# Performance work log

Hardware: AMD Instinct MI355X
Metric: run time of the kernel (lower is better)

## Reference

```python
import jax, jax.numpy as jnp
import numpy as np

SEG_LENS = (2048, 4096, 8192)
DIL_RATES = (1, 2, 4)
NUM_HEADS = 12
HEAD_DIM = 64
LN_EPS = 1e-5


def _dilated_attention(q, k, v):
    # q,k,v: [b, n, h, d]; heads partitioned across (segment, dilation) groups
    b, n, h, d = q.shape
    G = len(SEG_LENS)
    hg = h // G
    scale = d ** -0.5
    out = jnp.zeros_like(q)
    for i, (s, r) in enumerate(zip(SEG_LENS, DIL_RATES)):
        hmin = i * hg
        m = n // s                      # number of segments
        idx = jnp.arange(i % r, s, r)   # dilated positions within a segment, len = s // r
        def seg(t):
            # [b, n, hg, d] -> [b, m, s//r, hg, d]
            return t[:, :, hmin:hmin + hg, :].reshape(b, m, s, hg, d)[:, :, idx]
        qs, ks, vs = seg(q), seg(k), seg(v)
        scores = jnp.einsum('bmshd,bmthd->bmhst', qs, ks) * scale  # [b,m,hg,s/r,s/r]
        attn = jax.nn.softmax(scores, axis=-1)
        o = jnp.einsum('bmhst,bmthd->bmshd', attn, vs)              # [b,m,s/r,hg,d]
        pos = (jnp.arange(m)[:, None] * s + idx[None, :]).reshape(-1)
        out = out.at[:, pos, hmin:hmin + hg, :].set(o.reshape(b, -1, hg, d))
    return out


def setup_inputs() -> dict:
    key = jax.random.key(0)
    ks = jax.random.split(key, 4)
    E = NUM_HEADS * HEAD_DIM
    b, n = 1, 8192
    x = jax.random.normal(ks[0], (b, n, E), dtype=jnp.float32)
    w_qkv = jax.random.normal(ks[1], (3 * E, E), dtype=jnp.float32) * (E ** -0.5)
    b_qkv = jnp.zeros((3 * E,), dtype=jnp.float32)
    w_out = jax.random.normal(ks[2], (E, E), dtype=jnp.float32) * (E ** -0.5)
    b_out = jnp.zeros((E,), dtype=jnp.float32)
    ln_gamma = jnp.ones((E,), dtype=jnp.float32)
    ln_beta = jnp.zeros((E,), dtype=jnp.float32)
    return {'x': x, 'w_qkv': w_qkv, 'b_qkv': b_qkv, 'w_out': w_out,
            'b_out': b_out, 'ln_gamma': ln_gamma, 'ln_beta': ln_beta}


def reference(x, w_qkv, b_qkv, w_out, b_out, ln_gamma, ln_beta):
    b, n, E = x.shape
    qkv = x @ w_qkv.T + b_qkv
    q, k, v = jnp.split(qkv, 3, axis=-1)
    shp = (b, n, NUM_HEADS, HEAD_DIM)
    o = _dilated_attention(q.reshape(shp), k.reshape(shp), v.reshape(shp)).reshape(b, n, E)
    # MAGNETO: LayerNorm on attention output before out projection
    mu = jnp.mean(o, axis=-1, keepdims=True)
    var = jnp.mean(jnp.square(o - mu), axis=-1, keepdims=True)
    on = (o - mu) / jnp.sqrt(var + LN_EPS) * ln_gamma + ln_beta
    return on @ w_out.T + b_out
```

## Files before the change

### kernel.cpp

```cpp
#include <hip/hip_runtime.h>
#include <hip/hip_bf16.h>
#include <cstdint>
#include <cstddef>


typedef __attribute__((ext_vector_type(8))) short short8;
typedef __attribute__((ext_vector_type(4))) short short4_;
typedef __attribute__((ext_vector_type(4))) float float4_;
typedef __attribute__((ext_vector_type(16))) float floatx16;
typedef __attribute__((ext_vector_type(4))) int int4_;

#if __has_builtin(__builtin_amdgcn_exp2f)
#define EXP2(x) __builtin_amdgcn_exp2f(x)
#else
#define EXP2(x) exp2f(x)
#endif

__device__ __forceinline__ float bf2f(short s) {
    unsigned int u = ((unsigned int)(unsigned short)s) << 16;
    float f;
    __builtin_memcpy(&f, &u, 4);
    return f;
}
__device__ __forceinline__ short f2bf(float f) {
    unsigned int u;
    __builtin_memcpy(&u, &f, 4);
    u += 0x7fffu + ((u >> 16) & 1u);
    return (short)(u >> 16);
}
__device__ __forceinline__ short8 f8_to_bf8(const float* __restrict__ p) {
    float4_ a = *(const float4_*)(p);
    float4_ b = *(const float4_*)(p + 4);
    short8 r;
    r[0] = f2bf(a[0]); r[1] = f2bf(a[1]); r[2] = f2bf(a[2]); r[3] = f2bf(a[3]);
    r[4] = f2bf(b[0]); r[5] = f2bf(b[1]); r[6] = f2bf(b[2]); r[7] = f2bf(b[3]);
    return r;
}
__device__ __forceinline__ void gll16(const short* g, short* l) {
    __builtin_amdgcn_global_load_lds(
        (const __attribute__((address_space(1))) unsigned int*)g,
        (__attribute__((address_space(3))) unsigned int*)l, 16, 0, 0);
}
__device__ __forceinline__ int cvtpk(float lo, float hi) {
    int r;
    asm("v_cvt_pk_bf16_f32 %0, %1, %2" : "=v"(r) : "v"(lo), "v"(hi));
    return r;
}

#define LDT 72

__global__ __launch_bounds__(256) void cvt3(
    const float* __restrict__ a, int na, const float* __restrict__ b, int nb,
    const float* __restrict__ c, int nc,
    short* __restrict__ oa, short* __restrict__ ob, short* __restrict__ oc)
{
    int i = (blockIdx.x * 256 + threadIdx.x) * 8;
    if (i < na) {
        *(short8*)&oa[i] = f8_to_bf8(a + i);
    } else if (i < na + nb) {
        int j = i - na;
        *(short8*)&ob[j] = f8_to_bf8(b + j);
    } else {
        int j = i - na - nb;
        if (j < nc) *(short8*)&oc[j] = f8_to_bf8(c + j);
    }
}

template<int EPI>
__global__ __launch_bounds__(256) void gemm128(
    const short* __restrict__ A, int lda,
    const short* __restrict__ B,
    const float* __restrict__ bias,
    void* __restrict__ Cv,
    int N, int K)
{
    __shared__ short As[128 * 64];
    __shared__ short Bs[128 * 64];
    const int tid  = threadIdx.x;
    const int wave = tid >> 6, lane = tid & 63;
    const int quad = lane >> 4, l16 = lane & 15;
    const int wr = wave >> 1, wc = wave & 1;
    const int m0 = blockIdx.y * 128, n0 = blockIdx.x * 128;
    const int lrow   = lane >> 3;
    const int lchunk = (lane & 7) ^ lrow;

    const short* Abase = A + (size_t)(m0 + wave * 32 + lrow) * lda + lchunk * 8;
    const short* Bbase = B + (size_t)(n0 + wave * 32 + lrow) * (size_t)K + lchunk * 8;
    short* AsW = &As[(wave * 32) * 64];
    short* BsW = &Bs[(wave * 32) * 64];

    float4_ acc[4][4] = {};

    for (int k0 = 0; k0 < K; k0 += 64) {
        __syncthreads();
        #pragma unroll
        for (int i = 0; i < 4; i++) {
            gll16(Abase + (size_t)(i * 8) * lda + k0, AsW + (i * 8) * 64);
            gll16(Bbase + (size_t)(i * 8) * K   + k0, BsW + (i * 8) * 64);
        }
        __syncthreads();
        #pragma unroll
        for (int ks = 0; ks < 2; ks++) {
            short8 af[4], bf[4];
            const int ca = ((ks * 4 + quad) ^ (l16 & 7)) * 8;
            #pragma unroll
            for (int t = 0; t < 4; t++) {
                af[t] = *(const short8*)&As[(wr * 64 + t * 16 + l16) * 64 + ca];
                bf[t] = *(const short8*)&Bs[(wc * 64 + t * 16 + l16) * 64 + ca];
            }
            #pragma unroll
            for (int mt = 0; mt < 4; mt++)
                #pragma unroll
                for (int nt = 0; nt < 4; nt++)
                    acc[mt][nt] = __builtin_amdgcn_mfma_f32_16x16x32_bf16(
                        af[mt], bf[nt], acc[mt][nt], 0, 0, 0);
        }
    }

    #pragma unroll
    for (int nt = 0; nt < 4; nt++) {
        const int col = n0 + wc * 64 + nt * 16 + l16;
        const float bv = bias[col];
        if constexpr (EPI == 0) {
            short* C = (short*)Cv;
            const int g = col >> 8;
            #pragma unroll
            for (int mt = 0; mt < 4; mt++) {
                #pragma unroll
                for (int r = 0; r < 4; r++) {
                    int row = m0 + wr * 64 + mt * 16 + quad * 4 + r;
                    bool cov = (col >= 768) || (g == 0) ||
                               (g == 1 && (row & 1) == 1) ||
                               (g == 2 && (row & 3) == 2);
                    C[(size_t)row * N + col] = cov ? f2bf(acc[mt][nt][r] + bv) : (short)0;
                }
            }
        } else {
            float* C = (float*)Cv;
            #pragma unroll
            for (int mt = 0; mt < 4; mt++)
                #pragma unroll
                for (int r = 0; r < 4; r++) {
                    int row = m0 + wr * 64 + mt * 16 + quad * 4 + r;
                    C[(size_t)row * N + col] = acc[mt][nt][r] + bv;
                }
        }
    }
}

__global__ __launch_bounds__(256, 3) void dilated_attn(
    short* __restrict__ qkv, float* __restrict__ lbuf)
{
    __shared__ short Ks[2 * 64 * 64];
    __shared__ short Vt[2 * 64 * LDT];

    const int bx = blockIdx.x;
    const int L  = (bx & 7) * 56 + (bx >> 3);
    const int qt = L & 15;
    const int sh = L >> 4;

    int g, seg, s, rate, off0;
    if (sh < 16)      { g = 0; seg = sh >> 2;        s = 2048; rate = 1; off0 = 0; }
    else if (sh < 24) { g = 1; seg = (sh - 16) >> 2; s = 4096; rate = 2; off0 = 1; }
    else              { g = 2; seg = 0;              s = 8192; rate = 4; off0 = 2; }
    const int head = g * 4 + (sh & 3);

    const int tid  = threadIdx.x;
    const int wave = tid >> 6, lane = tid & 63;
    const int h = lane >> 5, l32 = lane & 31;
    const int srow = tid >> 2, scol = (tid & 3) * 16;

    const size_t bpos = (size_t)seg * s + off0
                      + (size_t)(qt * 128 + wave * 32) * rate;
    short8 aq[4];
    {
        const short* qsrc = qkv + (bpos + (size_t)l32 * rate) * 2304
                                + head * 64 + h * 8;
        #pragma unroll
        for (int kt = 0; kt < 4; kt++) {
            short8 q = *(const short8*)(qsrc + kt * 16);
            #pragma unroll
            for (int e = 0; e < 8; e++) q[e] = f2bf(bf2f(q[e]) * 0.1803368801111244f);
            aq[kt] = q;
        }
    }

    const int krow0  = wave * 8 + (lane >> 3);
    const int kchunk = (lane & 7) ^ (lane >> 3);
    const size_t kstep = (size_t)64 * rate * 2304;
    const short* kg0 = qkv + ((size_t)seg * s + off0 + (size_t)krow0 * rate) * 2304
                           + 768 + head * 64 + kchunk * 8;
    const short* kg1 = kg0 + (size_t)32 * rate * 2304;
    const short* vgp = qkv + ((size_t)seg * s + off0 + (size_t)srow * rate) * 2304
                           + 1536 + head * 64 + scol;
    const int kofsA = (wave * 8) * 64;
    const int kofsB = kofsA + 32 * 64;
    const int vswz  = scol;

    gll16(kg0, &Ks[kofsA]);
    gll16(kg1, &Ks[kofsB]);
    kg0 += kstep; kg1 += kstep;
    short8 va0 = *(const short8*)(vgp);
    short8 va1 = *(const short8*)(vgp + 8);
    vgp += kstep;
    #pragma unroll
    for (int e = 0; e < 8; e++) Vt[(scol + e) * LDT + (srow ^ vswz)] = va0[e];
    #pragma unroll
    for (int e = 0; e < 8; e++) Vt[(scol + 8 + e) * LDT + (srow ^ vswz)] = va1[e];
    va0 = *(const short8*)(vgp);
    va1 = *(const short8*)(vgp + 8);
    vgp += kstep;

    float lsum = 0.f;
    floatx16 oacc[2] = {};

    for (int j = 0; j < 32; j++) {
        __syncthreads();
        if (j < 31) {
            const int nb = (j + 1) & 1;
            gll16(kg0, &Ks[nb * 4096 + kofsA]);
            gll16(kg1, &Ks[nb * 4096 + kofsB]);
            kg0 += kstep; kg1 += kstep;
            short* vt = &Vt[nb * 64 * LDT];
            #pragma unroll
            for (int e = 0; e < 8; e++) vt[(scol + e) * LDT + (srow ^ vswz)] = va0[e];
            #pragma unroll
            for (int e = 0; e < 8; e++) vt[(scol + 8 + e) * LDT + (srow ^ vswz)] = va1[e];
            if (j < 30) {
                va0 = *(const short8*)(vgp);
                va1 = *(const short8*)(vgp + 8);
                vgp += kstep;
            }
        }
        const short* kb = &Ks[(j & 1) * 4096];
        const short* vb = &Vt[(j & 1) * 64 * LDT];

        floatx16 sacc[2] = {};
        __builtin_amdgcn_s_setprio(1);
        #pragma unroll
        for (int kt = 0; kt < 4; kt++) {
            #pragma unroll
            for (int t = 0; t < 2; t++) {
                short8 ak = *(const short8*)&kb[(t * 32 + l32) * 64
                                                + (((kt * 2 + h) ^ (l32 & 7)) * 8)];
                sacc[t] = __builtin_amdgcn_mfma_f32_32x32x16_bf16(
                    ak, aq[kt], sacc[t], 0, 0, 0);
            }
        }
        __builtin_amdgcn_s_setprio(0);

        #pragma unroll
        for (int e = 0; e < 16; e++) {
            float pa_ = EXP2(sacc[0][e]);
            float pb_ = EXP2(sacc[1][e]);
            sacc[0][e] = pa_; sacc[1][e] = pb_;
            lsum += pa_ + pb_;
        }

        short8 pa[4];
        #pragma unroll
        for (int kt = 0; kt < 4; kt++) {
            const int t = kt >> 1, b = (kt & 1) * 8;
            int A1 = cvtpk(sacc[t][b + 0], sacc[t][b + 1]);
            int A2 = cvtpk(sacc[t][b + 2], sacc[t][b + 3]);
            int B1 = cvtpk(sacc[t][b + 4], sacc[t][b + 5]);
            int B2 = cvtpk(sacc[t][b + 6], sacc[t][b + 7]);
            asm volatile("v_permlane32_swap_b32 %0, %1" : "+v"(A1), "+v"(B1));
            asm volatile("v_permlane32_swap_b32 %0, %1" : "+v"(A2), "+v"(B2));
            int4_ w; w[0] = A1; w[1] = A2; w[2] = B1; w[3] = B2;
            __builtin_memcpy(&pa[kt], &w, 16);
        }

        __builtin_amdgcn_s_setprio(1);
        #pragma unroll
        for (int kt = 0; kt < 4; kt++) {
            #pragma unroll
            for (int dt = 0; dt < 2; dt++) {
                const int d = dt * 32 + l32;
                short8 bv = *(const short8*)&vb[d * LDT
                                                + ((kt ^ ((d >> 4) & 3)) * 16 + h * 8)];
                oacc[dt] = __builtin_amdgcn_mfma_f32_32x32x16_bf16(
                    pa[kt], bv, oacc[dt], 0, 0, 0);
            }
        }
        __builtin_amdgcn_s_setprio(0);
    }

    {
        float lt = lsum + __shfl_xor(lsum, 32, 64);
        #pragma unroll
        for (int m = 0; m < 4; m++) {
            #pragma unroll
            for (int r = 0; r < 4; r++) {
                const int ql = 4 * h + r + 8 * m;
                short* od = qkv + (bpos + (size_t)ql * rate) * 2304 + head * 64;
                od[l32]      = f2bf(oacc[0][m * 4 + r]);
                od[32 + l32] = f2bf(oacc[1][m * 4 + r]);
            }
        }
        if (lane < 32)
            lbuf[(bpos + (size_t)l32 * rate) * 12 + head] = lt;
    }
}

__global__ __launch_bounds__(256) void ln_inplace(
    short* __restrict__ qkv, const float* __restrict__ lbuf,
    const float* __restrict__ gamma, const float* __restrict__ beta)
{
    const int row  = blockIdx.x * 4 + (threadIdx.x >> 6);
    const int lane = threadIdx.x & 63;
    short* src = qkv + (size_t)row * 2304;

    const int h1 = lane >> 3;
    const int h2 = 8 + (lane >> 4);
    const bool cov1 = (h1 < 4) || ((row & 1) == 1);
    const bool cov2 = ((row & 3) == 2);
    const float li1 = cov1 ? 1.0f / lbuf[row * 12 + h1] : 0.0f;
    const float li2 = cov2 ? 1.0f / lbuf[row * 12 + h2] : 0.0f;

    short8  a = *(const short8*)&src[lane * 8];
    short4_ b = *(const short4_*)&src[512 + lane * 4];
    float v[12];
    #pragma unroll
    for (int e = 0; e < 8; e++) v[e] = bf2f(a[e]) * li1;
    #pragma unroll
    for (int e = 0; e < 4; e++) v[8 + e] = bf2f(b[e]) * li2;

    float sum = 0.f, sq = 0.f;
    #pragma unroll
    for (int e = 0; e < 12; e++) { sum += v[e]; sq += v[e] * v[e]; }
    #pragma unroll
    for (int off = 1; off < 64; off <<= 1) {
        sum += __shfl_xor(sum, off, 64);
        sq  += __shfl_xor(sq,  off, 64);
    }
    float mean = sum * (1.0f / 768.0f);
    float var  = sq * (1.0f / 768.0f) - mean * mean;
    float rstd = rsqrtf(var + 1e-5f);

    short8 o8; short4_ o4;
    #pragma unroll
    for (int e = 0; e < 8; e++)
        o8[e] = f2bf((v[e] - mean) * rstd * gamma[lane * 8 + e] + beta[lane * 8 + e]);
    #pragma unroll
    for (int e = 0; e < 4; e++)
        o4[e] = f2bf((v[8 + e] - mean) * rstd * gamma[512 + lane * 4 + e] + beta[512 + lane * 4 + e]);

    *(short8*)&src[lane * 8] = o8;
    *(short4_*)&src[512 + lane * 4] = o4;
}

extern "C" void kernel_launch(void* const* d_in, const int* in_sizes, int n_in,
                              void* d_out, int out_size, void* d_ws, size_t ws_size,
                              hipStream_t stream) {
    const float* x     = (const float*)d_in[0];
    const float* w_qkv = (const float*)d_in[1];
    const float* b_qkv = (const float*)d_in[2];
    const float* w_out = (const float*)d_in[3];
    const float* b_out = (const float*)d_in[4];
    const float* gamma = (const float*)d_in[5];
    const float* beta  = (const float*)d_in[6];
    float* out = (float*)d_out;

    const int NX = 8192 * 768, NW1 = 2304 * 768, NW2 = 768 * 768;
    char* ws = (char*)d_ws;
    short* qkv   = (short*)(ws);
    short* xb    = (short*)(ws + (size_t)8192 * 2304 * 2);
    short* wqkvb = xb + NX;
    short* woutb = wqkvb + NW1;
    float* lbuf  = (float*)(woutb + NW2);

    cvt3<<<dim3((NX + NW1 + NW2) / (256 * 8)), 256, 0, stream>>>(
        x, NX, w_qkv, NW1, w_out, NW2, xb, wqkvb, woutb);

    gemm128<0><<<dim3(2304 / 128, 8192 / 128), 256, 0, stream>>>(
        xb, 768, wqkvb, b_qkv, qkv, 2304, 768);

    dilated_attn<<<dim3(28 * 16), 256, 0, stream>>>(qkv, lbuf);

    ln_inplace<<<dim3(8192 / 4), 256, 0, stream>>>(qkv, lbuf, gamma, beta);

    gemm128<1><<<dim3(768 / 128, 8192 / 128), 256, 0, stream>>>(
        qkv, 2304, woutb, b_out, out, 768, 768);
}
```

Before: 213.4 us.

## Split attention key range into two halves and merge partial sums in LayerNorm

The attention kernel now splits each query tile's key/value sweep into two halves handled by separate blocks. This doubles the grid from 448 to 896 blocks and raises the launch-bounds occupancy hint from 3 to 4, to fill the GPU better. Each half writes an unnormalized partial output to its own buffer (one reuses the x conversion area) and its own row-sum buffer. The LayerNorm kernel then adds the two partials and divides by the combined sum. The cost is extra global writes and reads of the partial outputs, and the merge relies on both halves sharing the same softmax offset.

Result: faster. 207.7 us (-2.7%).

```diff
diff --git a/kernel.cpp b/kernel.cpp
--- a/kernel.cpp
+++ b/kernel.cpp
@@ -148,16 +148,18 @@
     }
 }
 
-__global__ __launch_bounds__(256, 3) void dilated_attn(
-    short* __restrict__ qkv, float* __restrict__ lbuf)
+__global__ __launch_bounds__(256, 4) void dilated_attn(
+    const short* __restrict__ qkv, short* __restrict__ obuf1,
+    short* __restrict__ obuf2, float* __restrict__ lbuf)
 {
     __shared__ short Ks[2 * 64 * 64];
     __shared__ short Vt[2 * 64 * LDT];
 
     const int bx = blockIdx.x;
-    const int L  = (bx & 7) * 56 + (bx >> 3);
-    const int qt = L & 15;
-    const int sh = L >> 4;
+    const int L  = (bx & 7) * 112 + (bx >> 3);
+    const int qt   = L & 15;
+    const int half = (L >> 4) & 1;
+    const int sh   = L >> 5;
 
     int g, seg, s, rate, off0;
     if (sh < 16)      { g = 0; seg = sh >> 2;        s = 2048; rate = 1; off0 = 0; }
@@ -188,10 +190,11 @@
     const int krow0  = wave * 8 + (lane >> 3);
     const int kchunk = (lane & 7) ^ (lane >> 3);
     const size_t kstep = (size_t)64 * rate * 2304;
-    const short* kg0 = qkv + ((size_t)seg * s + off0 + (size_t)krow0 * rate) * 2304
+    const size_t kq0 = (size_t)seg * s + off0 + (size_t)(half * 1024) * rate;
+    const short* kg0 = qkv + (kq0 + (size_t)krow0 * rate) * 2304
                            + 768 + head * 64 + kchunk * 8;
     const short* kg1 = kg0 + (size_t)32 * rate * 2304;
-    const short* vgp = qkv + ((size_t)seg * s + off0 + (size_t)srow * rate) * 2304
+    const short* vgp = qkv + (kq0 + (size_t)srow * rate) * 2304
                            + 1536 + head * 64 + scol;
     const int kofsA = (wave * 8) * 64;
     const int kofsB = kofsA + 32 * 64;
@@ -214,9 +217,9 @@
     float lsum = 0.f;
     floatx16 oacc[2] = {};
 
-    for (int j = 0; j < 32; j++) {
+    for (int j = 0; j < 16; j++) {
         __syncthreads();
-        if (j < 31) {
+        if (j < 15) {
             const int nb = (j + 1) & 1;
             gll16(kg0, &Ks[nb * 4096 + kofsA]);
             gll16(kg1, &Ks[nb * 4096 + kofsB]);
@@ -226,7 +229,7 @@
             for (int e = 0; e < 8; e++) vt[(scol + e) * LDT + (srow ^ vswz)] = va0[e];
             #pragma unroll
             for (int e = 0; e < 8; e++) vt[(scol + 8 + e) * LDT + (srow ^ vswz)] = va1[e];
-            if (j < 30) {
+            if (j < 14) {
                 va0 = *(const short8*)(vgp);
                 va1 = *(const short8*)(vgp + 8);
                 vgp += kstep;
@@ -287,44 +290,55 @@
     }
 
     {
+        short* obase = half ? obuf2 : obuf1;
+        float* lb = lbuf + (size_t)half * 8192 * 12;
         float lt = lsum + __shfl_xor(lsum, 32, 64);
         #pragma unroll
         for (int m = 0; m < 4; m++) {
             #pragma unroll
             for (int r = 0; r < 4; r++) {
                 const int ql = 4 * h + r + 8 * m;
-                short* od = qkv + (bpos + (size_t)ql * rate) * 2304 + head * 64;
+                short* od = obase + (bpos + (size_t)ql * rate) * 768 + head * 64;
                 od[l32]      = f2bf(oacc[0][m * 4 + r]);
                 od[32 + l32] = f2bf(oacc[1][m * 4 + r]);
             }
         }
         if (lane < 32)
-            lbuf[(bpos + (size_t)l32 * rate) * 12 + head] = lt;
+            lb[(bpos + (size_t)l32 * rate) * 12 + head] = lt;
     }
 }
 
 __global__ __launch_bounds__(256) void ln_inplace(
-    short* __restrict__ qkv, const float* __restrict__ lbuf,
+    short* __restrict__ qkv, const short* __restrict__ obuf1,
+    const short* __restrict__ obuf2, const float* __restrict__ lbuf,
     const float* __restrict__ gamma, const float* __restrict__ beta)
 {
     const int row  = blockIdx.x * 4 + (threadIdx.x >> 6);
     const int lane = threadIdx.x & 63;
-    short* src = qkv + (size_t)row * 2304;
+    const short* s1 = obuf1 + (size_t)row * 768;
+    const short* s2 = obuf2 + (size_t)row * 768;
+    short* dst = qkv + (size_t)row * 2304;
 
     const int h1 = lane >> 3;
     const int h2 = 8 + (lane >> 4);
     const bool cov1 = (h1 < 4) || ((row & 1) == 1);
     const bool cov2 = ((row & 3) == 2);
-    const float li1 = cov1 ? 1.0f / lbuf[row * 12 + h1] : 0.0f;
-    const float li2 = cov2 ? 1.0f / lbuf[row * 12 + h2] : 0.0f;
-
-    short8  a = *(const short8*)&src[lane * 8];
-    short4_ b = *(const short4_*)&src[512 + lane * 4];
+    const float li1 = cov1
+        ? 1.0f / (lbuf[row * 12 + h1] + lbuf[8192 * 12 + row * 12 + h1]) : 0.0f;
+    const float li2 = cov2
+        ? 1.0f / (lbuf[row * 12 + h2] + lbuf[8192 * 12 + row * 12 + h2]) : 0.0f;
+
+    short8  a  = *(const short8*)&s1[lane * 8];
+    short4_ b  = *(const short4_*)&s1[512 + lane * 4];
+    short8  a2 = *(const short8*)&s2[lane * 8];
+    short4_ b2 = *(const short4_*)&s2[512 + lane * 4];
     float v[12];
     #pragma unroll
-    for (int e = 0; e < 8; e++) v[e] = bf2f(a[e]) * li1;
-    #pragma unroll
-    for (int e = 0; e < 4; e++) v[8 + e] = bf2f(b[e]) * li2;
+    for (int e = 0; e < 8; e++)
+        v[e] = cov1 ? (bf2f(a[e]) + bf2f(a2[e])) * li1 : 0.0f;
+    #pragma unroll
+    for (int e = 0; e < 4; e++)
+        v[8 + e] = cov2 ? (bf2f(b[e]) + bf2f(b2[e])) * li2 : 0.0f;
 
     float sum = 0.f, sq = 0.f;
     #pragma unroll
@@ -346,8 +360,8 @@
     for (int e = 0; e < 4; e++)
         o4[e] = f2bf((v[8 + e] - mean) * rstd * gamma[512 + lane * 4 + e] + beta[512 + lane * 4 + e]);
 
-    *(short8*)&src[lane * 8] = o8;
-    *(short4_*)&src[512 + lane * 4] = o4;
+    *(short8*)&dst[lane * 8] = o8;
+    *(short4_*)&dst[512 + lane * 4] = o4;
 }
 
 extern "C" void kernel_launch(void* const* d_in, const int* in_sizes, int n_in,
@@ -369,6 +383,8 @@
     short* wqkvb = xb + NX;
     short* woutb = wqkvb + NW1;
     float* lbuf  = (float*)(woutb + NW2);
+    short* obuf2 = (short*)(lbuf + 2 * 8192 * 12);
+    short* obuf1 = xb;
 
     cvt3<<<dim3((NX + NW1 + NW2) / (256 * 8)), 256, 0, stream>>>(
         x, NX, w_qkv, NW1, w_out, NW2, xb, wqkvb, woutb);
@@ -376,9 +392,10 @@
     gemm128<0><<<dim3(2304 / 128, 8192 / 128), 256, 0, stream>>>(
         xb, 768, wqkvb, b_qkv, qkv, 2304, 768);
 
-    dilated_attn<<<dim3(28 * 16), 256, 0, stream>>>(qkv, lbuf);
-
-    ln_inplace<<<dim3(8192 / 4), 256, 0, stream>>>(qkv, lbuf, gamma, beta);
+    dilated_attn<<<dim3(28 * 2 * 16), 256, 0, stream>>>(qkv, obuf1, obuf2, lbuf);
+
+    ln_inplace<<<dim3(8192 / 4), 256, 0, stream>>>(
+        qkv, obuf1, obuf2, lbuf, gamma, beta);
 
     gemm128<1><<<dim3(768 / 128, 8192 / 128), 256, 0, stream>>>(
         qkv, 2304, woutb, b_out, out, 768, 768);
```
